# Optimization experiments

Hardware: AMD Instinct MI355X
Metric: run time of the kernel (lower is better)

The kernel has to match this reference:

```python
import jax, jax.numpy as jnp
import numpy as np

EPS = 1e-8

def setup_inputs() -> dict:
    key = jax.random.key(0)
    ks = jax.random.split(key, 8)
    B, D, N, F = 8192, 1024, 2048, 8
    d2 = D // 2
    # integer-valued data (IDF acts on integers)
    x = jnp.round(jax.random.normal(ks[0], (B, D), jnp.float32) * 5.0)
    s1 = 1.0 / np.sqrt(d2)
    s2 = 1.0 / np.sqrt(N)
    return {
        "x": x,
        "W1": jax.random.normal(ks[1], (F, d2, N), jnp.float32) * s1,
        "b1": jax.random.normal(ks[2], (F, N), jnp.float32) * 0.01,
        "W2": jax.random.normal(ks[3], (F, N, N), jnp.float32) * s2,
        "b2": jax.random.normal(ks[4], (F, N), jnp.float32) * 0.01,
        "W3": jax.random.normal(ks[5], (F, N, d2), jnp.float32) * s2,
        "b3": jax.random.normal(ks[6], (F, d2), jnp.float32) * 0.01,
        "mean": jnp.zeros((1, D), jnp.float32),
        "log_scale": jnp.ones((1, D), jnp.float32),
    }

def _st_round(v):
    # straight-through round: forward round, identity gradient
    return v + jax.lax.stop_gradient(jnp.round(v) - v)

def _flow(x, W1, b1, W2, b2, W3, b3):
    d2 = x.shape[1] // 2
    def step(z, p):
        w1, bb1, w2, bb2, w3, bb3 = p
        xa, xb = z[:, :d2], z[:, d2:]
        h = jax.nn.leaky_relu(xa @ w1 + bb1)          # [B, N]
        h = jax.nn.leaky_relu(h @ w2 + bb2)           # [B, N]
        t = h @ w3 + bb3                               # [B, d2]
        yb = xb + _st_round(t)
        z = jnp.concatenate([xa, yb], axis=1)[:, ::-1]  # coupling + flip permute
        return z, None
    z, _ = jax.lax.scan(step, x, (W1, b1, W2, b2, W3, b3))
    return z

def reference(x, W1, b1, W2, b2, W3, b3, mean, log_scale):
    z = _flow(x, W1, b1, W2, b2, W3, b3)
    # discretized logistic log-prior: log(sig((z+.5-m)/s) - sig((z-.5-m)/s))
    scale = jnp.exp(log_scale)
    la = jax.nn.log_sigmoid((z + 0.5 - mean) / scale)
    lb = jax.nn.log_sigmoid((z - 0.5 - mean) / scale)
    log_p = la + jnp.log(1.0 - jnp.exp(lb - la) + EPS)  # log_min_exp
    return -log_p.sum(axis=1).mean()  # reduction='avg'
```

## Files before the change

kernel.cpp:

```cpp
#include <hip/hip_runtime.h>
#include <hip/hip_bf16.h>
#include <cmath>


typedef __bf16 bf16_t;
typedef bf16_t bf16x8 __attribute__((ext_vector_type(8)));
typedef float floatx4 __attribute__((ext_vector_type(4)));

#define BQ 8192
#define DD 1024
#define D2 512
#define NH 2048
#define NF 8

__device__ __forceinline__ void gload_lds16(const void* g, void* l) {
    __builtin_amdgcn_global_load_lds(
        (__attribute__((address_space(1))) void*)g,
        (__attribute__((address_space(3))) void*)l, 16, 0, 0);
}

__global__ __launch_bounds__(256)
void transpose_bf16(const float* __restrict__ W, bf16_t* __restrict__ Wt,
                    int K, int N) {
    __shared__ float tile[32][33];
    size_t fo = (size_t)blockIdx.z * K * N;
    int n0 = blockIdx.x * 32, k0 = blockIdx.y * 32;
    int tx = threadIdx.x & 31, ty = threadIdx.x >> 5;
    for (int i = 0; i < 4; i++)
        tile[ty + i*8][tx] = W[fo + (size_t)(k0 + ty + i*8) * N + n0 + tx];
    __syncthreads();
    for (int i = 0; i < 4; i++)
        Wt[fo + (size_t)(n0 + ty + i*8) * K + k0 + tx] = (bf16_t)tile[tx][ty + i*8];
}

__global__ __launch_bounds__(256)
void copy_x(const float4* __restrict__ x, float4* __restrict__ S) {
    int idx = blockIdx.x * blockDim.x + threadIdx.x;
    S[idx] = x[idx];
}

__global__ __launch_bounds__(256)
void prep_A(const float* __restrict__ S, bf16_t* __restrict__ Ab) {
    int idx = blockIdx.x * blockDim.x + threadIdx.x;
    int m = idx >> 9;
    int j = idx & 511;
    Ab[idx] = (bf16_t)S[(size_t)m * DD + j];
}

template<int MODE, int K, int TM, int TN, int MINW>
__global__ __launch_bounds__(256, MINW)
void gemm_kernel(const bf16_t* __restrict__ A, const bf16_t* __restrict__ Bt,
                 const float* __restrict__ bias,
                 bf16_t* __restrict__ Cout, float* __restrict__ S,
                 bf16_t* __restrict__ Abn,
                 int N, int rflag)
{
    constexpr int IM   = TM / 32;
    constexpr int JN   = TN / 32;
    constexpr int NA   = TM / 64;
    constexpr int NBD  = TN / 64;
    constexpr int NDMA = NA + NBD;
    constexpr int T    = K / 32;
    static_assert((T - 1) % 3 == 0, "pipeline triple-unroll needs (T-1)%3==0");
    static_assert(JN % 4 == 0, "bff processed in groups of 4");

    __shared__ __align__(16) bf16_t As[3][TM * 32];
    __shared__ __align__(16) bf16_t Bs[3][TN * 32];

    const int tid  = threadIdx.x;
    const int lane = tid & 63;
    const int wave = tid >> 6;
    const int wm   = wave >> 1;
    const int wn   = wave & 1;
    const int m0   = blockIdx.y * TM;
    const int n0   = blockIdx.x * TN;

    const int srow = tid >> 2;
    const int sq   = ((tid & 3) ^ ((srow >> 1) & 3)) * 8;
    const bf16_t* agp = A  + (size_t)(m0 + srow) * K + sq;
    const bf16_t* bgp = Bt + (size_t)(n0 + srow) * K + sq;

    floatx4 acc[IM][JN];
#pragma unroll
    for (int i = 0; i < IM; i++)
#pragma unroll
        for (int j = 0; j < JN; j++)
            acc[i][j] = (floatx4){0.f, 0.f, 0.f, 0.f};

    const int fr  = lane & 15;
    const int fp8 = ((lane >> 4) ^ ((lane >> 1) & 3)) * 8;

#define ISSUE_TILE(NB)                                                       \
    {                                                                        \
        _Pragma("unroll")                                                    \
        for (int u = 0; u < NA; u++)                                         \
            gload_lds16(agp + (size_t)(u*64) * K, &As[NB][u*2048 + tid*8]);  \
        _Pragma("unroll")                                                    \
        for (int u = 0; u < NBD; u++)                                        \
            gload_lds16(bgp + (size_t)(u*64) * K, &Bs[NB][u*2048 + tid*8]);  \
        agp += 32; bgp += 32;                                                \
    }

#define COMPUTE(CB)                                                          \
    {                                                                        \
        bf16x8 af[IM];                                                       \
        _Pragma("unroll")                                                    \
        for (int i = 0; i < IM; i++)                                         \
            af[i] = *(const bf16x8*)&As[CB][(wm*(TM/2) + i*16 + fr)*32 + fp8];\
        _Pragma("unroll")                                                    \
        for (int g2 = 0; g2 < JN/4; g2++) {                                  \
            bf16x8 bff[4];                                                   \
            _Pragma("unroll")                                                \
            for (int j = 0; j < 4; j++)                                      \
                bff[j] = *(const bf16x8*)                                    \
                    &Bs[CB][(wn*(TN/2) + (g2*4+j)*16 + fr)*32 + fp8];        \
            _Pragma("unroll")                                                \
            for (int i = 0; i < IM; i++)                                     \
                _Pragma("unroll")                                            \
                for (int j = 0; j < 4; j++)                                  \
                    acc[i][g2*4+j] = __builtin_amdgcn_mfma_f32_16x16x32_bf16(\
                                    af[i], bff[j], acc[i][g2*4+j], 0, 0, 0); \
        }                                                                    \
    }

#define PIPE_STEP(NB, CB)                                                    \
    {                                                                        \
        ISSUE_TILE(NB);                                                      \
        __builtin_amdgcn_s_waitcnt(0x0F70 | NDMA);     \
        __builtin_amdgcn_s_barrier();                                        \
        COMPUTE(CB);                                                         \
    }

    ISSUE_TILE(0);

#pragma unroll 1
    for (int g = 0; g < (T - 1) / 3; ++g) {
        PIPE_STEP(1, 0);
        PIPE_STEP(2, 1);
        PIPE_STEP(0, 2);
    }
    __builtin_amdgcn_s_waitcnt(0x0F70);
    __builtin_amdgcn_s_barrier();
    COMPUTE(0);

#undef PIPE_STEP
#undef COMPUTE
#undef ISSUE_TILE

    const int ccol  = lane & 15;
    const int crow4 = (lane >> 4) * 4;
#pragma unroll
    for (int j = 0; j < JN; j++) {
        int col = n0 + wn*(TN/2) + j*16 + ccol;
        float bj = bias[col];
        if (MODE == 0) {
#pragma unroll
            for (int i = 0; i < IM; i++) {
#pragma unroll
                for (int r = 0; r < 4; r++) {
                    int row = m0 + wm*(TM/2) + i*16 + crow4 + r;
                    float v = acc[i][j][r] + bj;
                    v = v >= 0.f ? v : 0.01f * v;
                    Cout[(size_t)row * N + col] = (bf16_t)v;
                }
            }
        } else {
            int slot = rflag ? (511 - col) : (512 + col);
            int aj   = 511 - col;
#pragma unroll
            for (int i = 0; i < IM; i++) {
#pragma unroll
                for (int r = 0; r < 4; r++) {
                    int row = m0 + wm*(TM/2) + i*16 + crow4 + r;
                    float t = acc[i][j][r] + bj;
                    float nv = S[(size_t)row * DD + slot] + rintf(t);
                    S[(size_t)row * DD + slot] = nv;
                    Abn[(size_t)row * D2 + aj] = (bf16_t)nv;
                }
            }
        }
    }
}

template<int K>
__global__ __launch_bounds__(512, 2)
void gemm256_kernel(const bf16_t* __restrict__ A, const bf16_t* __restrict__ Bt,
                    const float* __restrict__ bias, bf16_t* __restrict__ Cout,
                    int N)
{
    constexpr int T = K / 64;
    static_assert(T >= 4, "pipeline needs >=4 K-tiles");

    __shared__ __align__(16) bf16_t As[2][16384];
    __shared__ __align__(16) bf16_t Bs[2][16384];

    const int tid  = threadIdx.x;
    const int lane = tid & 63;
    const int wave = tid >> 6;
    const int wm   = wave >> 2;
    const int wn   = wave & 3;
    const int m0   = blockIdx.y * 256;
    const int n0   = blockIdx.x * 256;

    const int srow = tid >> 3;
    const int sq   = ((tid & 7) ^ (srow & 7)) * 8;
    const bf16_t* agp = A  + (size_t)(m0 + srow) * K + sq;
    const bf16_t* bgp = Bt + (size_t)(n0 + srow) * K + sq;
    const int ldst = tid * 8;

#define STAGE_A(H, TILE, BUF)                                                 \
    {                                                                         \
        _Pragma("unroll")                                                     \
        for (int u = 0; u < 2; ++u)                                           \
            gload_lds16(agp + (size_t)((H)*128 + u*64) * K + (size_t)(TILE)*64,\
                        &As[BUF][(H)*8192 + u*4096 + ldst]);                  \
    }
#define STAGE_B(H, TILE, BUF)                                                 \
    {                                                                         \
        _Pragma("unroll")                                                     \
        for (int u = 0; u < 2; ++u)                                           \
            gload_lds16(bgp + (size_t)((H)*128 + u*64) * K + (size_t)(TILE)*64,\
                        &Bs[BUF][(H)*8192 + u*4096 + ldst]);                  \
    }
#define MFMA16(D, Av, Bv) \
    D = __builtin_amdgcn_mfma_f32_16x16x32_bf16(Av, Bv, D, 0, 0, 0)

    floatx4 acc[8][4];
#pragma unroll
    for (int i = 0; i < 8; ++i)
#pragma unroll
        for (int j = 0; j < 4; ++j)
            acc[i][j] = (floatx4){0.f, 0.f, 0.f, 0.f};

    const int fr = lane & 15;
    const int l7 = lane & 7;
    const int qh = lane >> 4;
    const int ra = (wm*128 + fr) * 64;
    const int rb = (wn*64  + fr) * 64;
    const int c0 = ((qh    ) ^ l7) * 8;
    const int c1 = ((qh + 4) ^ l7) * 8;

    STAGE_B(0, 0, 0); STAGE_B(1, 0, 0);
    STAGE_A(0, 0, 0); STAGE_A(1, 0, 0);
    STAGE_B(0, 1, 1); STAGE_B(1, 1, 1);
    __builtin_amdgcn_s_waitcnt(0x0F74);
    __builtin_amdgcn_s_barrier();

#pragma unroll 1
    for (int tau = 0; tau < T; ++tau) {
        const int c = tau & 1;
        const bf16_t* Ac = As[c];
        const bf16_t* Bc = Bs[c];
        bf16x8 af[4][2], b01[2][2], b23[2][2];

#pragma unroll
        for (int i = 0; i < 4; ++i) {
            af[i][0] = *(const bf16x8*)&Ac[ra + i*1024 + c0];
            af[i][1] = *(const bf16x8*)&Ac[ra + i*1024 + c1];
        }
#pragma unroll
        for (int j = 0; j < 2; ++j) {
            b01[j][0] = *(const bf16x8*)&Bc[rb + j*1024 + c0];
            b01[j][1] = *(const bf16x8*)&Bc[rb + j*1024 + c1];
        }
        if (tau + 1 < T) STAGE_A(0, tau + 1, c ^ 1);
        __builtin_amdgcn_s_barrier();
        __builtin_amdgcn_s_setprio(1);
#pragma unroll
        for (int i = 0; i < 4; ++i)
#pragma unroll
            for (int j = 0; j < 2; ++j) {
                MFMA16(acc[i][j], af[i][0], b01[j][0]);
                MFMA16(acc[i][j], af[i][1], b01[j][1]);
            }
        __builtin_amdgcn_s_setprio(0);
        __builtin_amdgcn_s_barrier();

#pragma unroll
        for (int j = 0; j < 2; ++j) {
            b23[j][0] = *(const bf16x8*)&Bc[rb + (j+2)*1024 + c0];
            b23[j][1] = *(const bf16x8*)&Bc[rb + (j+2)*1024 + c1];
        }
        if (tau + 1 < T) STAGE_A(1, tau + 1, c ^ 1);
        __builtin_amdgcn_s_barrier();
        __builtin_amdgcn_s_setprio(1);
#pragma unroll
        for (int i = 0; i < 4; ++i)
#pragma unroll
            for (int j = 0; j < 2; ++j) {
                MFMA16(acc[i][j+2], af[i][0], b23[j][0]);
                MFMA16(acc[i][j+2], af[i][1], b23[j][1]);
            }
        __builtin_amdgcn_s_setprio(0);
        __builtin_amdgcn_s_barrier();

#pragma unroll
        for (int i = 0; i < 4; ++i) {
            af[i][0] = *(const bf16x8*)&Ac[ra + (i+4)*1024 + c0];
            af[i][1] = *(const bf16x8*)&Ac[ra + (i+4)*1024 + c1];
        }
        if (tau + 2 < T) STAGE_B(0, tau + 2, c);
        __builtin_amdgcn_s_barrier();
        __builtin_amdgcn_s_setprio(1);
#pragma unroll
        for (int i = 0; i < 4; ++i)
#pragma unroll
            for (int j = 0; j < 2; ++j) {
                MFMA16(acc[i+4][j+2], af[i][0], b23[j][0]);
                MFMA16(acc[i+4][j+2], af[i][1], b23[j][1]);
            }
        __builtin_amdgcn_s_setprio(0);
        __builtin_amdgcn_s_barrier();

        if (tau + 2 < T) STAGE_B(1, tau + 2, c);
        __builtin_amdgcn_s_barrier();
        __builtin_amdgcn_s_setprio(1);
#pragma unroll
        for (int i = 0; i < 4; ++i)
#pragma unroll
            for (int j = 0; j < 2; ++j) {
                MFMA16(acc[i+4][j], af[i][0], b01[j][0]);
                MFMA16(acc[i+4][j], af[i][1], b01[j][1]);
            }
        __builtin_amdgcn_s_setprio(0);
        if (tau < T - 2)       __builtin_amdgcn_s_waitcnt(0x0F74);
        else if (tau == T - 2) __builtin_amdgcn_s_waitcnt(0x0F70);
        __builtin_amdgcn_s_barrier();
    }

#undef STAGE_A
#undef STAGE_B
#undef MFMA16

    const int ccol  = lane & 15;
    const int crow4 = (lane >> 4) * 4;
#pragma unroll
    for (int j = 0; j < 4; ++j) {
        int col = n0 + wn*64 + j*16 + ccol;
        float bj = bias[col];
#pragma unroll
        for (int i = 0; i < 8; ++i) {
#pragma unroll
            for (int r = 0; r < 4; ++r) {
                int row = m0 + wm*128 + i*16 + crow4 + r;
                float v = acc[i][j][r] + bj;
                v = v >= 0.f ? v : 0.01f * v;
                Cout[(size_t)row * N + col] = (bf16_t)v;
            }
        }
    }
}

__global__ __launch_bounds__(256)
void reduce_nll(const float* __restrict__ S, const float* __restrict__ mean,
                const float* __restrict__ log_scale, float* __restrict__ out)
{
    float local = 0.f;
    const int total = BQ * DD;
    for (int idx = blockIdx.x * blockDim.x + threadIdx.x; idx < total;
         idx += gridDim.x * blockDim.x) {
        int j = idx & (DD - 1);
        float z  = S[idx];
        float mu = mean[j];
        float sc = expf(log_scale[j]);
        float ua = (z + 0.5f - mu) / sc;
        float ub = (z - 0.5f - mu) / sc;
        float la = fminf(ua, 0.f) - log1pf(expf(-fabsf(ua)));
        float lb = fminf(ub, 0.f) - log1pf(expf(-fabsf(ub)));
        float lp = la + logf(1.0f - expf(lb - la) + 1e-8f);
        local += lp;
    }
    __shared__ float red[256];
    red[threadIdx.x] = local;
    __syncthreads();
    for (int s = 128; s > 0; s >>= 1) {
        if (threadIdx.x < s) red[threadIdx.x] += red[threadIdx.x + s];
        __syncthreads();
    }
    if (threadIdx.x == 0) atomicAdd(out, -red[0] * (1.0f / (float)BQ));
}

extern "C" void kernel_launch(void* const* d_in, const int* in_sizes, int n_in,
                              void* d_out, int out_size, void* d_ws, size_t ws_size,
                              hipStream_t stream)
{
    const float* x   = (const float*)d_in[0];
    const float* W1  = (const float*)d_in[1];
    const float* b1  = (const float*)d_in[2];
    const float* W2  = (const float*)d_in[3];
    const float* b2  = (const float*)d_in[4];
    const float* W3  = (const float*)d_in[5];
    const float* b3  = (const float*)d_in[6];
    const float* mean = (const float*)d_in[7];
    const float* lsc  = (const float*)d_in[8];

    char* ws = (char*)d_ws;
    bf16_t* Wt1 = (bf16_t*)ws; ws += (size_t)NF * NH * D2 * 2;
    bf16_t* Wt2 = (bf16_t*)ws; ws += (size_t)NF * NH * NH * 2;
    bf16_t* Wt3 = (bf16_t*)ws; ws += (size_t)NF * D2 * NH * 2;
    float*  S   = (float*)ws;  ws += (size_t)BQ * DD * 4;
    bf16_t* Ab  = (bf16_t*)ws; ws += (size_t)BQ * D2 * 2;
    bf16_t* H1  = (bf16_t*)ws; ws += (size_t)BQ * NH * 2;
    bf16_t* H2  = (bf16_t*)ws;

    hipMemsetAsync(d_out, 0, sizeof(float), stream);

    dim3 blk(256);
    transpose_bf16<<<dim3(NH/32, D2/32, NF), blk, 0, stream>>>(W1, Wt1, D2, NH);
    transpose_bf16<<<dim3(NH/32, NH/32, NF), blk, 0, stream>>>(W2, Wt2, NH, NH);
    transpose_bf16<<<dim3(D2/32, NH/32, NF), blk, 0, stream>>>(W3, Wt3, NH, D2);

    copy_x<<<BQ * DD / 4 / 256, blk, 0, stream>>>((const float4*)x, (float4*)S);
    prep_A<<<BQ * D2 / 256, blk, 0, stream>>>(S, Ab);

    for (int f = 0; f < NF; ++f) {
        int r = f & 1;
        gemm256_kernel<D2><<<dim3(NH/256, BQ/256), dim3(512), 0, stream>>>(
            Ab, Wt1 + (size_t)f * NH * D2, b1 + (size_t)f * NH, H1, NH);
        gemm256_kernel<NH><<<dim3(NH/256, BQ/256), dim3(512), 0, stream>>>(
            H1, Wt2 + (size_t)f * NH * NH, b2 + (size_t)f * NH, H2, NH);
        gemm_kernel<1, NH, 64, 128, 3><<<dim3(D2/128, BQ/64), blk, 0, stream>>>(
            H2, Wt3 + (size_t)f * D2 * NH, b3 + (size_t)f * D2, nullptr, S,
            Ab, D2, r);
    }

    reduce_nll<<<2048, blk, 0, stream>>>(S, mean, lsc, (float*)d_out);
}
```

Measured before the change: 1.602 ms.

## Restructure GEMM pipeline to prefetch A two tiles ahead and preload B fragments

Reschedules the LDS staging in the 256x256 GEMM main loop so that both A halves are loaded two K-tiles ahead, as B already was. The B01 fragments for the next tile are read at the end of each iteration instead of at the start. Explicit lgkmcnt(0) fences and sched_barriers pin the ordering of LDS reads ahead of the MFMA blocks. The aim is to hide global-to-LDS latency and LDS read latency behind MFMA work. In exchange, more loads are in flight and the vmcnt bookkeeping is more intricate, so a wrong count could cause races.

Result: slower. 1.766 ms (+10.2%).

```diff
diff --git a/kernel.cpp b/kernel.cpp
--- a/kernel.cpp
+++ b/kernel.cpp
@@ -182,6 +182,12 @@
     }
 }
 
+#define LGKM0_FENCE()                                        \
+    {                                                        \
+        asm volatile("s_waitcnt lgkmcnt(0)" ::: "memory");   \
+        __builtin_amdgcn_sched_barrier(0);                   \
+    }
+
 template<int K>
 __global__ __launch_bounds__(512, 2)
 void gemm256_kernel(const bf16_t* __restrict__ A, const bf16_t* __restrict__ Bt,
@@ -242,29 +248,34 @@
 
     STAGE_B(0, 0, 0); STAGE_B(1, 0, 0);
     STAGE_A(0, 0, 0); STAGE_A(1, 0, 0);
-    STAGE_B(0, 1, 1); STAGE_B(1, 1, 1);
-    __builtin_amdgcn_s_waitcnt(0x0F74);
+    STAGE_B(0, 1, 1);
+    STAGE_A(0, 1, 1); STAGE_A(1, 1, 1); STAGE_B(1, 1, 1);
+    __builtin_amdgcn_s_waitcnt(0x0F78);
     __builtin_amdgcn_s_barrier();
+    __builtin_amdgcn_sched_barrier(0);
+
+    bf16x8 b01[2][2];
+#pragma unroll
+    for (int j = 0; j < 2; ++j) {
+        b01[j][0] = *(const bf16x8*)&Bs[0][rb + j*1024 + c0];
+        b01[j][1] = *(const bf16x8*)&Bs[0][rb + j*1024 + c1];
+    }
 
 #pragma unroll 1
     for (int tau = 0; tau < T; ++tau) {
         const int c = tau & 1;
         const bf16_t* Ac = As[c];
         const bf16_t* Bc = Bs[c];
-        bf16x8 af[4][2], b01[2][2], b23[2][2];
+        const bf16_t* Bn = Bs[c ^ 1];
+        bf16x8 af[4][2], b23[2][2];
 
 #pragma unroll
         for (int i = 0; i < 4; ++i) {
             af[i][0] = *(const bf16x8*)&Ac[ra + i*1024 + c0];
             af[i][1] = *(const bf16x8*)&Ac[ra + i*1024 + c1];
         }
-#pragma unroll
-        for (int j = 0; j < 2; ++j) {
-            b01[j][0] = *(const bf16x8*)&Bc[rb + j*1024 + c0];
-            b01[j][1] = *(const bf16x8*)&Bc[rb + j*1024 + c1];
-        }
-        if (tau + 1 < T) STAGE_A(0, tau + 1, c ^ 1);
-        __builtin_amdgcn_s_barrier();
+        __builtin_amdgcn_s_barrier();
+        LGKM0_FENCE();
         __builtin_amdgcn_s_setprio(1);
 #pragma unroll
         for (int i = 0; i < 4; ++i)
@@ -281,8 +292,8 @@
             b23[j][0] = *(const bf16x8*)&Bc[rb + (j+2)*1024 + c0];
             b23[j][1] = *(const bf16x8*)&Bc[rb + (j+2)*1024 + c1];
         }
-        if (tau + 1 < T) STAGE_A(1, tau + 1, c ^ 1);
-        __builtin_amdgcn_s_barrier();
+        __builtin_amdgcn_s_barrier();
+        LGKM0_FENCE();
         __builtin_amdgcn_s_setprio(1);
 #pragma unroll
         for (int i = 0; i < 4; ++i)
@@ -301,6 +312,7 @@
         }
         if (tau + 2 < T) STAGE_B(0, tau + 2, c);
         __builtin_amdgcn_s_barrier();
+        LGKM0_FENCE();
         __builtin_amdgcn_s_setprio(1);
 #pragma unroll
         for (int i = 0; i < 4; ++i)
@@ -310,10 +322,17 @@
                 MFMA16(acc[i+4][j+2], af[i][1], b23[j][1]);
             }
         __builtin_amdgcn_s_setprio(0);
-        __builtin_amdgcn_s_barrier();
-
-        if (tau + 2 < T) STAGE_B(1, tau + 2, c);
-        __builtin_amdgcn_s_barrier();
+        if (tau < T - 2) __builtin_amdgcn_s_waitcnt(0x0F72);
+        else             __builtin_amdgcn_s_waitcnt(0x0F70);
+        __builtin_amdgcn_s_barrier();
+
+        if (tau + 2 < T) {
+            STAGE_A(0, tau + 2, c);
+            STAGE_A(1, tau + 2, c);
+            STAGE_B(1, tau + 2, c);
+        }
+        __builtin_amdgcn_s_barrier();
+        LGKM0_FENCE();
         __builtin_amdgcn_s_setprio(1);
 #pragma unroll
         for (int i = 0; i < 4; ++i)
@@ -323,8 +342,14 @@
                 MFMA16(acc[i+4][j], af[i][1], b01[j][1]);
             }
         __builtin_amdgcn_s_setprio(0);
-        if (tau < T - 2)       __builtin_amdgcn_s_waitcnt(0x0F74);
-        else if (tau == T - 2) __builtin_amdgcn_s_waitcnt(0x0F70);
+        if (tau + 1 < T) {
+#pragma unroll
+            for (int j = 0; j < 2; ++j) {
+                b01[j][0] = *(const bf16x8*)&Bn[rb + j*1024 + c0];
+                b01[j][1] = *(const bf16x8*)&Bn[rb + j*1024 + c1];
+            }
+        }
+        __builtin_amdgcn_sched_barrier(0);
         __builtin_amdgcn_s_barrier();
     }
 
```
